# Kernel tuning notes

Hardware: AMD Instinct MI355X
Metric: run time of the kernel (lower is better)

## Reference

```python
import jax, jax.numpy as jnp
import numpy as np

N = 30000      # nodes
E = 480000     # edges (no self loops; GATConv adds them)
IN = 256       # in_features
OUT = 128      # out_features == per-head channels (concat=False)
H = 4          # heads
NEG_SLOPE = 0.2


def setup_inputs() -> dict:
    key = jax.random.key(0)
    k = jax.random.split(key, 6)
    x = jax.random.normal(k[0], (N, IN), dtype=jnp.float32)
    src = jax.random.randint(k[1], (E,), 0, N, dtype=jnp.int32)
    # guarantee no self loops (GATConv would strip them before re-adding)
    off = jax.random.randint(k[2], (E,), 1, N, dtype=jnp.int32)
    dst = (src + off) % N
    edge_index = jnp.stack([src, dst])  # [2, E]
    W = jax.random.normal(k[3], (IN, H * OUT), dtype=jnp.float32) / np.float32(np.sqrt(IN))
    att_src = jax.random.normal(k[4], (H, OUT), dtype=jnp.float32) / np.float32(np.sqrt(OUT))
    att_dst = jax.random.normal(k[5], (H, OUT), dtype=jnp.float32) / np.float32(np.sqrt(OUT))
    bias = jnp.zeros((OUT,), dtype=jnp.float32)
    return {"x": x, "edge_index": edge_index, "W": W,
            "att_src": att_src, "att_dst": att_dst, "bias": bias}


def reference(x, edge_index, W, att_src, att_dst, bias):
    n = x.shape[0]
    # dense projection -> per-head features [N, H, C]
    h = (x @ W).reshape(n, H, OUT)
    a_s = jnp.einsum('nhc,hc->nh', h, att_src)  # [N, H]
    a_d = jnp.einsum('nhc,hc->nh', h, att_dst)  # [N, H]
    # add self loops (GATConv default add_self_loops=True)
    loop = jnp.arange(n, dtype=edge_index.dtype)
    src = jnp.concatenate([edge_index[0], loop])  # [Et]
    dst = jnp.concatenate([edge_index[1], loop])  # [Et]
    # per-edge attention logits + LeakyReLU
    alpha = jax.nn.leaky_relu(a_s[src] + a_d[dst], NEG_SLOPE)  # [Et, H]
    # segment softmax over incoming edges of each dst node
    amax = jax.ops.segment_max(alpha, dst, num_segments=n)      # [N, H]
    ex = jnp.exp(alpha - amax[dst])
    denom = jax.ops.segment_sum(ex, dst, num_segments=n)        # [N, H]
    w = ex / denom[dst]                                          # [Et, H]
    # gather source features, weight, scatter-add to dst
    msg = h[src] * w[:, :, None]                                 # [Et, H, C]
    out = jax.ops.segment_sum(msg, dst, num_segments=n)          # [N, H, C]
    # concat=False -> mean over heads, then bias, then module's tanh
    out = out.mean(axis=1) + bias                                # [N, C]
    return jnp.tanh(out)
```

## Files before the change

### kernel.cpp

```cpp
#include <hip/hip_runtime.h>
#include <math.h>

#define IN_F   256
#define OUT_F  128
#define HEADS  4
#define HD     (HEADS * OUT_F)
#define NEG    0.2f
#define CAP    64

typedef __attribute__((ext_vector_type(8))) short short8;
typedef __attribute__((ext_vector_type(4))) float f32x4;

static __device__ __forceinline__ ushort f2bf(float f) {
    union { float f; unsigned u; } v; v.f = f;
    unsigned r = (v.u + 0x7FFFu + ((v.u >> 16) & 1u)) >> 16;
    return (ushort)r;
}
static __device__ __forceinline__ float bflo(unsigned u) {
    union { unsigned u; float f; } v; v.u = u << 16; return v.f;
}
static __device__ __forceinline__ float bfhi(unsigned u) {
    union { unsigned u; float f; } v; v.u = u & 0xFFFF0000u; return v.f;
}

__global__ __launch_bounds__(256) void cvt_wt(const float* __restrict__ W,
                                              ushort* __restrict__ WT) {
    int idx = blockIdx.x * blockDim.x + threadIdx.x;
    int n = idx >> 8, k = idx & 255;
    WT[idx] = f2bf(W[k * HD + n]);
}
__global__ __launch_bounds__(256) void calc_va(const float* __restrict__ W,
                                               const float* __restrict__ att_src,
                                               const float* __restrict__ att_dst,
                                               float* __restrict__ va_s,
                                               float* __restrict__ va_d) {
    int idx = blockIdx.x * blockDim.x + threadIdx.x;
    int h = idx >> 8, k = idx & 255;
    const float* wr = W + (size_t)k * HD + h * OUT_F;
    const float* as = att_src + h * OUT_F;
    const float* ad = att_dst + h * OUT_F;
    float ss = 0.f, sd = 0.f;
#pragma unroll 8
    for (int c = 0; c < OUT_F; ++c) {
        float w = wr[c];
        ss = fmaf(w, as[c], ss);
        sd = fmaf(w, ad[c], sd);
    }
    va_s[idx] = ss;
    va_d[idx] = sd;
}

__global__ __launch_bounds__(256) void fused_x(const float* __restrict__ X,
                                               const float* __restrict__ va_s,
                                               const float* __restrict__ va_d,
                                               ushort* __restrict__ Xb,
                                               float* __restrict__ a_s,
                                               float* __restrict__ a_d,
                                               int n_nodes) {
    const int lane = threadIdx.x & 63;
    const int node = blockIdx.x * 4 + (threadIdx.x >> 6);
    if (node >= n_nodes) return;
    float4 v = *(const float4*)(X + (size_t)node * IN_F + lane * 4);
    ushort4 o; o.x = f2bf(v.x); o.y = f2bf(v.y); o.z = f2bf(v.z); o.w = f2bf(v.w);
    *(ushort4*)(Xb + (size_t)node * IN_F + lane * 4) = o;

    float ps[HEADS], pd[HEADS];
#pragma unroll
    for (int hd = 0; hd < HEADS; ++hd) {
        float4 s4 = *(const float4*)(va_s + hd * IN_F + lane * 4);
        float4 d4 = *(const float4*)(va_d + hd * IN_F + lane * 4);
        ps[hd] = v.x * s4.x + v.y * s4.y + v.z * s4.z + v.w * s4.w;
        pd[hd] = v.x * d4.x + v.y * d4.y + v.z * d4.z + v.w * d4.w;
    }
#pragma unroll
    for (int off = 32; off > 0; off >>= 1) {
#pragma unroll
        for (int hd = 0; hd < HEADS; ++hd) {
            ps[hd] += __shfl_xor(ps[hd], off, 64);
            pd[hd] += __shfl_xor(pd[hd], off, 64);
        }
    }
    if (lane == 0) {
        float4 s4 = make_float4(ps[0], ps[1], ps[2], ps[3]);
        float4 d4 = make_float4(pd[0], pd[1], pd[2], pd[3]);
        *(float4*)(a_s + node * 4) = s4;
        *(float4*)(a_d + node * 4) = d4;
    }
}

#define GBM 128
#define GBN 128
#define GBK 32
#define LDA 40

__global__ __launch_bounds__(256) void gemm_mfma(const ushort* __restrict__ Xb,
                                                 const ushort* __restrict__ WT,
                                                 ushort* __restrict__ Hb,
                                                 int n_nodes) {
    __shared__ ushort As[GBM][LDA];
    __shared__ ushort Bs[GBN][LDA];
    const int tid = threadIdx.x;
    const int m0 = blockIdx.y * GBM;
    const int n0 = blockIdx.x * GBN;
    const int wave = tid >> 6, lane = tid & 63;
    const int wm = (wave & 1) * 64, wn = (wave >> 1) * 64;
    const int l15 = lane & 15, quad = lane >> 4;

    f32x4 acc[4][4];
#pragma unroll
    for (int i = 0; i < 4; ++i)
#pragma unroll
        for (int j = 0; j < 4; ++j) acc[i][j] = (f32x4){0.f, 0.f, 0.f, 0.f};

    const int r = tid >> 2, q = tid & 3;

    for (int k0 = 0; k0 < IN_F; k0 += GBK) {
        uint4 a0 = make_uint4(0, 0, 0, 0), a1 = a0;
        int gm0 = m0 + r, gm1 = m0 + 64 + r;
        if (gm0 < n_nodes) a0 = *(const uint4*)(Xb + (size_t)gm0 * IN_F + k0 + q * 8);
        if (gm1 < n_nodes) a1 = *(const uint4*)(Xb + (size_t)gm1 * IN_F + k0 + q * 8);
        uint4 b0 = *(const uint4*)(WT + (size_t)(n0 + r) * IN_F + k0 + q * 8);
        uint4 b1 = *(const uint4*)(WT + (size_t)(n0 + 64 + r) * IN_F + k0 + q * 8);
        __syncthreads();
        *(uint4*)&As[r][q * 8] = a0;
        *(uint4*)&As[64 + r][q * 8] = a1;
        *(uint4*)&Bs[r][q * 8] = b0;
        *(uint4*)&Bs[64 + r][q * 8] = b1;
        __syncthreads();

        short8 af[4], bf_[4];
#pragma unroll
        for (int f = 0; f < 4; ++f) {
            af[f]  = *(const short8*)&As[wm + f * 16 + l15][quad * 8];
            bf_[f] = *(const short8*)&Bs[wn + f * 16 + l15][quad * 8];
        }
#pragma unroll
        for (int fm = 0; fm < 4; ++fm)
#pragma unroll
            for (int fn = 0; fn < 4; ++fn)
                acc[fm][fn] = __builtin_amdgcn_mfma_f32_16x16x32_bf16(
                    af[fm], bf_[fn], acc[fm][fn], 0, 0, 0);
    }

#pragma unroll
    for (int fm = 0; fm < 4; ++fm) {
        int gmb = m0 + wm + fm * 16 + quad * 4;
#pragma unroll
        for (int reg = 0; reg < 4; ++reg) {
            int gm = gmb + reg;
            if (gm < n_nodes) {
#pragma unroll
                for (int fn = 0; fn < 4; ++fn)
                    Hb[(size_t)gm * HD + n0 + wn + fn * 16 + l15] =
                        f2bf(acc[fm][fn][reg]);
            }
        }
    }
}

__global__ __launch_bounds__(256) void build_table(const int* __restrict__ src,
                                                   const int* __restrict__ dst,
                                                   int* __restrict__ cursor,
                                                   int* __restrict__ table,
                                                   int n_edges) {
    int e = blockIdx.x * blockDim.x + threadIdx.x;
    if (e >= n_edges) return;
    int d = dst[e];
    int r = atomicAdd(&cursor[d], 1);
    if (r < CAP) table[(size_t)d * CAP + r] = src[e];
}

__global__ __launch_bounds__(256) void prep_weights(const float* __restrict__ a_s,
                                                    const float* __restrict__ a_d,
                                                    const int* __restrict__ cursor,
                                                    const int* __restrict__ table,
                                                    float* __restrict__ wtab,
                                                    float* __restrict__ wself,
                                                    float* __restrict__ rden,
                                                    int n_nodes) {
    const int lane = threadIdx.x & 63;
    const int n = blockIdx.x * 4 + (threadIdx.x >> 6);
    if (n >= n_nodes) return;
    int deg = cursor[n]; if (deg > CAP) deg = CAP;
    const int* row = table + (size_t)n * CAP;
    const float4 ad4 = *(const float4*)(a_d + n * 4);
    const float4 as4 = *(const float4*)(a_s + n * 4);
    const float ad[4] = {ad4.x, ad4.y, ad4.z, ad4.w};

    float aself[4];
    {
        const float asn[4] = {as4.x, as4.y, as4.z, as4.w};
#pragma unroll
        for (int hd = 0; hd < 4; ++hd) {
            float al = asn[hd] + ad[hd];
            aself[hd] = al > 0.f ? al : NEG * al;
        }
    }
    const bool act = lane < deg;
    float al[4];
    {
        int s = act ? row[lane] : 0;
        float4 av = act ? *(const float4*)(a_s + s * 4) : make_float4(0.f, 0.f, 0.f, 0.f);
        const float as_[4] = {av.x, av.y, av.z, av.w};
#pragma unroll
        for (int hd = 0; hd < 4; ++hd) {
            float a = as_[hd] + ad[hd];
            a = a > 0.f ? a : NEG * a;
            al[hd] = act ? a : -1e30f;
        }
    }
    float m[4];
#pragma unroll
    for (int hd = 0; hd < 4; ++hd) m[hd] = al[hd];
#pragma unroll
    for (int off = 32; off > 0; off >>= 1)
#pragma unroll
        for (int hd = 0; hd < 4; ++hd)
            m[hd] = fmaxf(m[hd], __shfl_xor(m[hd], off, 64));
#pragma unroll
    for (int hd = 0; hd < 4; ++hd) m[hd] = fmaxf(m[hd], aself[hd]);

    float w[4], den[4];
#pragma unroll
    for (int hd = 0; hd < 4; ++hd) {
        w[hd] = act ? __expf(al[hd] - m[hd]) : 0.f;
        den[hd] = w[hd];
    }
#pragma unroll
    for (int off = 32; off > 0; off >>= 1)
#pragma unroll
        for (int hd = 0; hd < 4; ++hd)
            den[hd] += __shfl_xor(den[hd], off, 64);

    if (act)
        *(float4*)(wtab + ((size_t)n * CAP + lane) * 4) =
            make_float4(w[0], w[1], w[2], w[3]);
    if (lane == 0) {
        float es[4];
        float4 ws, rd;
#pragma unroll
        for (int hd = 0; hd < 4; ++hd) es[hd] = __expf(aself[hd] - m[hd]);
        ws = make_float4(es[0], es[1], es[2], es[3]);
        rd = make_float4(1.f / (den[0] + es[0]), 1.f / (den[1] + es[1]),
                         1.f / (den[2] + es[2]), 1.f / (den[3] + es[3]));
        *(float4*)(wself + n * 4) = ws;
        *(float4*)(rden + n * 4) = rd;
    }
}

__global__ __launch_bounds__(256) void gat_agg(const ushort* __restrict__ Hb,
                                               const float* __restrict__ wtab,
                                               const float* __restrict__ wself,
                                               const float* __restrict__ rden,
                                               const int* __restrict__ cursor,
                                               const int* __restrict__ table,
                                               const float* __restrict__ bias,
                                               float* __restrict__ out) {
    const int lane = threadIdx.x & 63;
    const int n = blockIdx.x * 4 + (threadIdx.x >> 6);
    if (n >= 30000) return;
    int deg = cursor[n]; if (deg > CAP) deg = CAP;
    const int* row = table + (size_t)n * CAP;
    const float* wrow = wtab + (size_t)n * CAP * 4;
    const unsigned* hbase = (const unsigned*)Hb;

    float acc0[4], acc1[4];
    {
        const float4 ws = *(const float4*)(wself + n * 4);
        const float wsv[4] = {ws.x, ws.y, ws.z, ws.w};
        const unsigned* p = hbase + (size_t)n * 256;
#pragma unroll
        for (int hd = 0; hd < 4; ++hd) {
            unsigned u = p[hd * 64 + lane];
            acc0[hd] = wsv[hd] * bflo(u);
            acc1[hd] = wsv[hd] * bfhi(u);
        }
    }
    int e = 0;
    for (; e + 4 <= deg; e += 4) {
        int4 r4 = *(const int4*)(row + e);
        float4 w0 = *(const float4*)(wrow + (e + 0) * 4);
        float4 w1 = *(const float4*)(wrow + (e + 1) * 4);
        float4 w2 = *(const float4*)(wrow + (e + 2) * 4);
        float4 w3 = *(const float4*)(wrow + (e + 3) * 4);
        const unsigned* p0 = hbase + (size_t)r4.x * 256;
        const unsigned* p1 = hbase + (size_t)r4.y * 256;
        const unsigned* p2 = hbase + (size_t)r4.z * 256;
        const unsigned* p3 = hbase + (size_t)r4.w * 256;
        unsigned u0[4], u1[4], u2[4], u3[4];
#pragma unroll
        for (int hd = 0; hd < 4; ++hd) {
            u0[hd] = p0[hd * 64 + lane];
            u1[hd] = p1[hd * 64 + lane];
            u2[hd] = p2[hd * 64 + lane];
            u3[hd] = p3[hd * 64 + lane];
        }
        const float wv0[4] = {w0.x, w0.y, w0.z, w0.w};
        const float wv1[4] = {w1.x, w1.y, w1.z, w1.w};
        const float wv2[4] = {w2.x, w2.y, w2.z, w2.w};
        const float wv3[4] = {w3.x, w3.y, w3.z, w3.w};
#pragma unroll
        for (int hd = 0; hd < 4; ++hd) {
            acc0[hd] = fmaf(wv0[hd], bflo(u0[hd]), acc0[hd]);
            acc1[hd] = fmaf(wv0[hd], bfhi(u0[hd]), acc1[hd]);
            acc0[hd] = fmaf(wv1[hd], bflo(u1[hd]), acc0[hd]);
            acc1[hd] = fmaf(wv1[hd], bfhi(u1[hd]), acc1[hd]);
            acc0[hd] = fmaf(wv2[hd], bflo(u2[hd]), acc0[hd]);
            acc1[hd] = fmaf(wv2[hd], bfhi(u2[hd]), acc1[hd]);
            acc0[hd] = fmaf(wv3[hd], bflo(u3[hd]), acc0[hd]);
            acc1[hd] = fmaf(wv3[hd], bfhi(u3[hd]), acc1[hd]);
        }
    }
    for (; e < deg; ++e) {
        int s = row[e];
        float4 w = *(const float4*)(wrow + e * 4);
        const float wv[4] = {w.x, w.y, w.z, w.w};
        const unsigned* p = hbase + (size_t)s * 256;
#pragma unroll
        for (int hd = 0; hd < 4; ++hd) {
            unsigned u = p[hd * 64 + lane];
            acc0[hd] = fmaf(wv[hd], bflo(u), acc0[hd]);
            acc1[hd] = fmaf(wv[hd], bfhi(u), acc1[hd]);
        }
    }
    const float4 rd = *(const float4*)(rden + n * 4);
    const float rdv[4] = {rd.x, rd.y, rd.z, rd.w};
    float o0 = 0.f, o1 = 0.f;
#pragma unroll
    for (int hd = 0; hd < 4; ++hd) {
        o0 = fmaf(acc0[hd], rdv[hd], o0);
        o1 = fmaf(acc1[hd], rdv[hd], o1);
    }
    float2 b = *(const float2*)(bias + 2 * lane);
    o0 = 0.25f * o0 + b.x;
    o1 = 0.25f * o1 + b.y;
    float2 ov = make_float2(tanhf(o0), tanhf(o1));
    *(float2*)(out + (size_t)n * OUT_F + 2 * lane) = ov;
}

extern "C" void kernel_launch(void* const* d_in, const int* in_sizes, int n_in,
                              void* d_out, int out_size, void* d_ws, size_t ws_size,
                              hipStream_t stream) {
    const float* x       = (const float*)d_in[0];
    const int*   ei      = (const int*)d_in[1];
    const float* W       = (const float*)d_in[2];
    const float* att_src = (const float*)d_in[3];
    const float* att_dst = (const float*)d_in[4];
    const float* bias    = (const float*)d_in[5];
    float* out = (float*)d_out;

    const int n_nodes = in_sizes[0] / IN_F;
    const int n_edges = in_sizes[1] / 2;
    const int* src = ei;
    const int* dst = ei + n_edges;

    char* ws = (char*)d_ws;
    size_t off = 0;
    auto alloc = [&](size_t bytes) -> void* {
        void* p = ws + off;
        off = (off + bytes + 255) & ~(size_t)255;
        return p;
    };
    ushort* Hb     = (ushort*)alloc((size_t)n_nodes * HD * sizeof(ushort));
    ushort* Xb     = (ushort*)alloc((size_t)n_nodes * IN_F * sizeof(ushort));
    ushort* WT     = (ushort*)alloc((size_t)HD * IN_F * sizeof(ushort));
    float*  va_s   = (float*)alloc((size_t)HEADS * IN_F * sizeof(float));
    float*  va_d   = (float*)alloc((size_t)HEADS * IN_F * sizeof(float));
    float*  a_s    = (float*)alloc((size_t)n_nodes * HEADS * sizeof(float));
    float*  a_d    = (float*)alloc((size_t)n_nodes * HEADS * sizeof(float));
    int*    cursor = (int*)alloc((size_t)n_nodes * sizeof(int));
    int*    table  = (int*)alloc((size_t)n_nodes * CAP * sizeof(int));
    float*  wtab   = (float*)alloc((size_t)n_nodes * CAP * 4 * sizeof(float));
    float*  wself  = (float*)alloc((size_t)n_nodes * 4 * sizeof(float));
    float*  rden   = (float*)alloc((size_t)n_nodes * 4 * sizeof(float));
    (void)ws_size; (void)n_in; (void)out_size;

    hipMemsetAsync(cursor, 0, (size_t)n_nodes * sizeof(int), stream);

    cvt_wt<<<(HD * IN_F) / 256, 256, 0, stream>>>(W, WT);
    calc_va<<<(HEADS * IN_F) / 256, 256, 0, stream>>>(W, att_src, att_dst, va_s, va_d);
    fused_x<<<(n_nodes + 3) / 4, 256, 0, stream>>>(x, va_s, va_d, Xb, a_s, a_d, n_nodes);
    build_table<<<(n_edges + 255) / 256, 256, 0, stream>>>(src, dst, cursor, table, n_edges);

    dim3 ggrid(HD / GBN, (n_nodes + GBM - 1) / GBM);
    gemm_mfma<<<ggrid, 256, 0, stream>>>(Xb, WT, Hb, n_nodes);

    prep_weights<<<(n_nodes + 3) / 4, 256, 0, stream>>>(a_s, a_d, cursor, table,
                                                        wtab, wself, rden, n_nodes);
    gat_agg<<<(n_nodes + 3) / 4, 256, 0, stream>>>(Hb, wtab, wself, rden, cursor, table,
                                                   bias, out);
}
```

Before: 235.7 us.

## Fuse softmax weight prep into aggregation and use direct global-to-LDS loads in GEMM

Merges the prep_weights kernel into gat_agg, so each wave computes the per-edge softmax weights in registers and broadcasts them with shuffles. This removes the wtab, wself and rden round trips through global memory and one kernel launch. The GEMM now stages tiles with global_load_lds and an XOR-swizzled, unpadded LDS layout to avoid the register staging and bank conflicts. The gather loop is widened to 8 edges per iteration. The GEMM drops its row bounds checks on A and relies on Xb being placed first in the workspace so that out-of-range reads of the last tile stay inside valid memory.

```diff
diff --git a/kernel.cpp b/kernel.cpp
--- a/kernel.cpp
+++ b/kernel.cpp
@@ -10,6 +10,9 @@
 
 typedef __attribute__((ext_vector_type(8))) short short8;
 typedef __attribute__((ext_vector_type(4))) float f32x4;
+
+typedef __attribute__((address_space(1))) const void* gp_t;
+typedef __attribute__((address_space(3))) void* lp_t;
 
 static __device__ __forceinline__ ushort f2bf(float f) {
     union { float f; unsigned u; } v; v.f = f;
@@ -91,14 +94,13 @@
 #define GBM 128
 #define GBN 128
 #define GBK 32
-#define LDA 40
 
 __global__ __launch_bounds__(256) void gemm_mfma(const ushort* __restrict__ Xb,
                                                  const ushort* __restrict__ WT,
                                                  ushort* __restrict__ Hb,
                                                  int n_nodes) {
-    __shared__ ushort As[GBM][LDA];
-    __shared__ ushort Bs[GBN][LDA];
+    __shared__ ushort As[GBM][GBK];
+    __shared__ ushort Bs[GBN][GBK];
     const int tid = threadIdx.x;
     const int m0 = blockIdx.y * GBM;
     const int n0 = blockIdx.x * GBN;
@@ -106,33 +108,39 @@
     const int wm = (wave & 1) * 64, wn = (wave >> 1) * 64;
     const int l15 = lane & 15, quad = lane >> 4;
 
+    const int rr = lane >> 2;
+    const int cg = (lane & 3) ^ ((lane >> 3) & 3);
+    const int rA = wave * 16 + rr;
+    const ushort* gA0 = Xb + (size_t)(m0 + rA) * IN_F + cg * 8;
+    const ushort* gA1 = Xb + (size_t)(m0 + 64 + rA) * IN_F + cg * 8;
+    const ushort* gB0 = WT + (size_t)(n0 + rA) * IN_F + cg * 8;
+    const ushort* gB1 = WT + (size_t)(n0 + 64 + rA) * IN_F + cg * 8;
+    ushort* lA0 = &As[wave * 16][0];
+    ushort* lA1 = &As[64 + wave * 16][0];
+    ushort* lB0 = &Bs[wave * 16][0];
+    ushort* lB1 = &Bs[64 + wave * 16][0];
+
     f32x4 acc[4][4];
 #pragma unroll
     for (int i = 0; i < 4; ++i)
 #pragma unroll
         for (int j = 0; j < 4; ++j) acc[i][j] = (f32x4){0.f, 0.f, 0.f, 0.f};
 
-    const int r = tid >> 2, q = tid & 3;
+    const int ks = (quad ^ ((l15 >> 1) & 3)) * 8;
 
     for (int k0 = 0; k0 < IN_F; k0 += GBK) {
-        uint4 a0 = make_uint4(0, 0, 0, 0), a1 = a0;
-        int gm0 = m0 + r, gm1 = m0 + 64 + r;
-        if (gm0 < n_nodes) a0 = *(const uint4*)(Xb + (size_t)gm0 * IN_F + k0 + q * 8);
-        if (gm1 < n_nodes) a1 = *(const uint4*)(Xb + (size_t)gm1 * IN_F + k0 + q * 8);
-        uint4 b0 = *(const uint4*)(WT + (size_t)(n0 + r) * IN_F + k0 + q * 8);
-        uint4 b1 = *(const uint4*)(WT + (size_t)(n0 + 64 + r) * IN_F + k0 + q * 8);
         __syncthreads();
-        *(uint4*)&As[r][q * 8] = a0;
-        *(uint4*)&As[64 + r][q * 8] = a1;
-        *(uint4*)&Bs[r][q * 8] = b0;
-        *(uint4*)&Bs[64 + r][q * 8] = b1;
+        __builtin_amdgcn_global_load_lds((gp_t)(gA0 + k0), (lp_t)lA0, 16, 0, 0);
+        __builtin_amdgcn_global_load_lds((gp_t)(gA1 + k0), (lp_t)lA1, 16, 0, 0);
+        __builtin_amdgcn_global_load_lds((gp_t)(gB0 + k0), (lp_t)lB0, 16, 0, 0);
+        __builtin_amdgcn_global_load_lds((gp_t)(gB1 + k0), (lp_t)lB1, 16, 0, 0);
         __syncthreads();
 
         short8 af[4], bf_[4];
 #pragma unroll
         for (int f = 0; f < 4; ++f) {
-            af[f]  = *(const short8*)&As[wm + f * 16 + l15][quad * 8];
-            bf_[f] = *(const short8*)&Bs[wn + f * 16 + l15][quad * 8];
+            af[f]  = *(const short8*)&As[wm + f * 16 + l15][ks];
+            bf_[f] = *(const short8*)&Bs[wn + f * 16 + l15][ks];
         }
 #pragma unroll
         for (int fm = 0; fm < 4; ++fm)
@@ -170,23 +178,24 @@
     if (r < CAP) table[(size_t)d * CAP + r] = src[e];
 }
 
-__global__ __launch_bounds__(256) void prep_weights(const float* __restrict__ a_s,
-                                                    const float* __restrict__ a_d,
-                                                    const int* __restrict__ cursor,
-                                                    const int* __restrict__ table,
-                                                    float* __restrict__ wtab,
-                                                    float* __restrict__ wself,
-                                                    float* __restrict__ rden,
-                                                    int n_nodes) {
+__global__ __launch_bounds__(256) void gat_agg(const ushort* __restrict__ Hb,
+                                               const float* __restrict__ a_s,
+                                               const float* __restrict__ a_d,
+                                               const int* __restrict__ cursor,
+                                               const int* __restrict__ table,
+                                               const float* __restrict__ bias,
+                                               float* __restrict__ out,
+                                               int n_nodes) {
     const int lane = threadIdx.x & 63;
     const int n = blockIdx.x * 4 + (threadIdx.x >> 6);
     if (n >= n_nodes) return;
     int deg = cursor[n]; if (deg > CAP) deg = CAP;
     const int* row = table + (size_t)n * CAP;
+    const unsigned* hbase = (const unsigned*)Hb;
+
     const float4 ad4 = *(const float4*)(a_d + n * 4);
     const float4 as4 = *(const float4*)(a_s + n * 4);
     const float ad[4] = {ad4.x, ad4.y, ad4.z, ad4.w};
-
     float aself[4];
     {
         const float asn[4] = {as4.x, as4.y, as4.z, as4.w};
@@ -200,7 +209,7 @@
     float al[4];
     {
         int s = act ? row[lane] : 0;
-        float4 av = act ? *(const float4*)(a_s + s * 4) : make_float4(0.f, 0.f, 0.f, 0.f);
+        float4 av = *(const float4*)(a_s + s * 4);
         const float as_[4] = {av.x, av.y, av.z, av.w};
 #pragma unroll
         for (int hd = 0; hd < 4; ++hd) {
@@ -220,7 +229,7 @@
 #pragma unroll
     for (int hd = 0; hd < 4; ++hd) m[hd] = fmaxf(m[hd], aself[hd]);
 
-    float w[4], den[4];
+    float w[4], den[4], es[4];
 #pragma unroll
     for (int hd = 0; hd < 4; ++hd) {
         w[hd] = act ? __expf(al[hd] - m[hd]) : 0.f;
@@ -231,100 +240,59 @@
 #pragma unroll
         for (int hd = 0; hd < 4; ++hd)
             den[hd] += __shfl_xor(den[hd], off, 64);
-
-    if (act)
-        *(float4*)(wtab + ((size_t)n * CAP + lane) * 4) =
-            make_float4(w[0], w[1], w[2], w[3]);
-    if (lane == 0) {
-        float es[4];
-        float4 ws, rd;
-#pragma unroll
-        for (int hd = 0; hd < 4; ++hd) es[hd] = __expf(aself[hd] - m[hd]);
-        ws = make_float4(es[0], es[1], es[2], es[3]);
-        rd = make_float4(1.f / (den[0] + es[0]), 1.f / (den[1] + es[1]),
-                         1.f / (den[2] + es[2]), 1.f / (den[3] + es[3]));
-        *(float4*)(wself + n * 4) = ws;
-        *(float4*)(rden + n * 4) = rd;
-    }
-}
-
-__global__ __launch_bounds__(256) void gat_agg(const ushort* __restrict__ Hb,
-                                               const float* __restrict__ wtab,
-                                               const float* __restrict__ wself,
-                                               const float* __restrict__ rden,
-                                               const int* __restrict__ cursor,
-                                               const int* __restrict__ table,
-                                               const float* __restrict__ bias,
-                                               float* __restrict__ out) {
-    const int lane = threadIdx.x & 63;
-    const int n = blockIdx.x * 4 + (threadIdx.x >> 6);
-    if (n >= 30000) return;
-    int deg = cursor[n]; if (deg > CAP) deg = CAP;
-    const int* row = table + (size_t)n * CAP;
-    const float* wrow = wtab + (size_t)n * CAP * 4;
-    const unsigned* hbase = (const unsigned*)Hb;
+    float rdv[4];
+#pragma unroll
+    for (int hd = 0; hd < 4; ++hd) {
+        es[hd] = __expf(aself[hd] - m[hd]);
+        rdv[hd] = 1.f / (den[hd] + es[hd]);
+    }
 
     float acc0[4], acc1[4];
     {
-        const float4 ws = *(const float4*)(wself + n * 4);
-        const float wsv[4] = {ws.x, ws.y, ws.z, ws.w};
         const unsigned* p = hbase + (size_t)n * 256;
 #pragma unroll
         for (int hd = 0; hd < 4; ++hd) {
             unsigned u = p[hd * 64 + lane];
-            acc0[hd] = wsv[hd] * bflo(u);
-            acc1[hd] = wsv[hd] * bfhi(u);
+            acc0[hd] = es[hd] * bflo(u);
+            acc1[hd] = es[hd] * bfhi(u);
         }
     }
     int e = 0;
-    for (; e + 4 <= deg; e += 4) {
-        int4 r4 = *(const int4*)(row + e);
-        float4 w0 = *(const float4*)(wrow + (e + 0) * 4);
-        float4 w1 = *(const float4*)(wrow + (e + 1) * 4);
-        float4 w2 = *(const float4*)(wrow + (e + 2) * 4);
-        float4 w3 = *(const float4*)(wrow + (e + 3) * 4);
-        const unsigned* p0 = hbase + (size_t)r4.x * 256;
-        const unsigned* p1 = hbase + (size_t)r4.y * 256;
-        const unsigned* p2 = hbase + (size_t)r4.z * 256;
-        const unsigned* p3 = hbase + (size_t)r4.w * 256;
-        unsigned u0[4], u1[4], u2[4], u3[4];
-#pragma unroll
-        for (int hd = 0; hd < 4; ++hd) {
-            u0[hd] = p0[hd * 64 + lane];
-            u1[hd] = p1[hd * 64 + lane];
-            u2[hd] = p2[hd * 64 + lane];
-            u3[hd] = p3[hd * 64 + lane];
-        }
-        const float wv0[4] = {w0.x, w0.y, w0.z, w0.w};
-        const float wv1[4] = {w1.x, w1.y, w1.z, w1.w};
-        const float wv2[4] = {w2.x, w2.y, w2.z, w2.w};
-        const float wv3[4] = {w3.x, w3.y, w3.z, w3.w};
-#pragma unroll
-        for (int hd = 0; hd < 4; ++hd) {
-            acc0[hd] = fmaf(wv0[hd], bflo(u0[hd]), acc0[hd]);
-            acc1[hd] = fmaf(wv0[hd], bfhi(u0[hd]), acc1[hd]);
-            acc0[hd] = fmaf(wv1[hd], bflo(u1[hd]), acc0[hd]);
-            acc1[hd] = fmaf(wv1[hd], bfhi(u1[hd]), acc1[hd]);
-            acc0[hd] = fmaf(wv2[hd], bflo(u2[hd]), acc0[hd]);
-            acc1[hd] = fmaf(wv2[hd], bfhi(u2[hd]), acc1[hd]);
-            acc0[hd] = fmaf(wv3[hd], bflo(u3[hd]), acc0[hd]);
-            acc1[hd] = fmaf(wv3[hd], bfhi(u3[hd]), acc1[hd]);
+    for (; e + 8 <= deg; e += 8) {
+        int4 ra = *(const int4*)(row + e);
+        int4 rb = *(const int4*)(row + e + 4);
+        const unsigned* p[8];
+        p[0] = hbase + (size_t)ra.x * 256; p[1] = hbase + (size_t)ra.y * 256;
+        p[2] = hbase + (size_t)ra.z * 256; p[3] = hbase + (size_t)ra.w * 256;
+        p[4] = hbase + (size_t)rb.x * 256; p[5] = hbase + (size_t)rb.y * 256;
+        p[6] = hbase + (size_t)rb.z * 256; p[7] = hbase + (size_t)rb.w * 256;
+        unsigned u[8][4];
+#pragma unroll
+        for (int j = 0; j < 8; ++j)
+#pragma unroll
+            for (int hd = 0; hd < 4; ++hd)
+                u[j][hd] = p[j][hd * 64 + lane];
+#pragma unroll
+        for (int j = 0; j < 8; ++j) {
+#pragma unroll
+            for (int hd = 0; hd < 4; ++hd) {
+                float wv = __shfl(w[hd], e + j, 64);
+                acc0[hd] = fmaf(wv, bflo(u[j][hd]), acc0[hd]);
+                acc1[hd] = fmaf(wv, bfhi(u[j][hd]), acc1[hd]);
+            }
         }
     }
     for (; e < deg; ++e) {
         int s = row[e];
-        float4 w = *(const float4*)(wrow + e * 4);
-        const float wv[4] = {w.x, w.y, w.z, w.w};
         const unsigned* p = hbase + (size_t)s * 256;
 #pragma unroll
         for (int hd = 0; hd < 4; ++hd) {
             unsigned u = p[hd * 64 + lane];
-            acc0[hd] = fmaf(wv[hd], bflo(u), acc0[hd]);
-            acc1[hd] = fmaf(wv[hd], bfhi(u), acc1[hd]);
-        }
-    }
-    const float4 rd = *(const float4*)(rden + n * 4);
-    const float rdv[4] = {rd.x, rd.y, rd.z, rd.w};
+            float wv = __shfl(w[hd], e, 64);
+            acc0[hd] = fmaf(wv, bflo(u), acc0[hd]);
+            acc1[hd] = fmaf(wv, bfhi(u), acc1[hd]);
+        }
+    }
     float o0 = 0.f, o1 = 0.f;
 #pragma unroll
     for (int hd = 0; hd < 4; ++hd) {
@@ -361,8 +329,8 @@
         off = (off + bytes + 255) & ~(size_t)255;
         return p;
     };
+    ushort* Xb     = (ushort*)alloc((size_t)n_nodes * IN_F * sizeof(ushort));
     ushort* Hb     = (ushort*)alloc((size_t)n_nodes * HD * sizeof(ushort));
-    ushort* Xb     = (ushort*)alloc((size_t)n_nodes * IN_F * sizeof(ushort));
     ushort* WT     = (ushort*)alloc((size_t)HD * IN_F * sizeof(ushort));
     float*  va_s   = (float*)alloc((size_t)HEADS * IN_F * sizeof(float));
     float*  va_d   = (float*)alloc((size_t)HEADS * IN_F * sizeof(float));
@@ -370,9 +338,6 @@
     float*  a_d    = (float*)alloc((size_t)n_nodes * HEADS * sizeof(float));
     int*    cursor = (int*)alloc((size_t)n_nodes * sizeof(int));
     int*    table  = (int*)alloc((size_t)n_nodes * CAP * sizeof(int));
-    float*  wtab   = (float*)alloc((size_t)n_nodes * CAP * 4 * sizeof(float));
-    float*  wself  = (float*)alloc((size_t)n_nodes * 4 * sizeof(float));
-    float*  rden   = (float*)alloc((size_t)n_nodes * 4 * sizeof(float));
     (void)ws_size; (void)n_in; (void)out_size;
 
     hipMemsetAsync(cursor, 0, (size_t)n_nodes * sizeof(int), stream);
@@ -385,8 +350,6 @@
     dim3 ggrid(HD / GBN, (n_nodes + GBM - 1) / GBM);
     gemm_mfma<<<ggrid, 256, 0, stream>>>(Xb, WT, Hb, n_nodes);
 
-    prep_weights<<<(n_nodes + 3) / 4, 256, 0, stream>>>(a_s, a_d, cursor, table,
-                                                        wtab, wself, rden, n_nodes);
-    gat_agg<<<(n_nodes + 3) / 4, 256, 0, stream>>>(Hb, wtab, wself, rden, cursor, table,
-                                                   bias, out);
-}
+    gat_agg<<<(n_nodes + 3) / 4, 256, 0, stream>>>(Hb, a_s, a_d, cursor, table,
+                                                   bias, out, n_nodes);
+}
```

Result: faster. 229.9 us (-2.5%).

## Load GEMM tiles directly into LDS with XOR swizzle; shrink aggregation blocks

Applied to the files above, without the earlier changes.

The GEMM now stages its A/B tiles with global_load_lds, which writes global data straight into shared memory and skips the register round-trip. The padded LDS layout is replaced by an XOR-swizzled one to avoid bank conflicts. The bounds check on rows is dropped, which is why Xb is now allocated before Hb, so the tail block's over-read of Xb lands in Hb's buffer instead of past the end. prep_weights and gat_agg move from 256-thread to 128-thread blocks, and gat_agg takes n_nodes as a parameter instead of a hardcoded count.

```diff
diff --git a/kernel.cpp b/kernel.cpp
--- a/kernel.cpp
+++ b/kernel.cpp
@@ -10,6 +10,9 @@
 
 typedef __attribute__((ext_vector_type(8))) short short8;
 typedef __attribute__((ext_vector_type(4))) float f32x4;
+
+typedef __attribute__((address_space(1))) const void* gp_t;
+typedef __attribute__((address_space(3))) void* lp_t;
 
 static __device__ __forceinline__ ushort f2bf(float f) {
     union { float f; unsigned u; } v; v.f = f;
@@ -91,14 +94,13 @@
 #define GBM 128
 #define GBN 128
 #define GBK 32
-#define LDA 40
 
 __global__ __launch_bounds__(256) void gemm_mfma(const ushort* __restrict__ Xb,
                                                  const ushort* __restrict__ WT,
                                                  ushort* __restrict__ Hb,
                                                  int n_nodes) {
-    __shared__ ushort As[GBM][LDA];
-    __shared__ ushort Bs[GBN][LDA];
+    __shared__ ushort As[GBM][GBK];
+    __shared__ ushort Bs[GBN][GBK];
     const int tid = threadIdx.x;
     const int m0 = blockIdx.y * GBM;
     const int n0 = blockIdx.x * GBN;
@@ -106,33 +108,39 @@
     const int wm = (wave & 1) * 64, wn = (wave >> 1) * 64;
     const int l15 = lane & 15, quad = lane >> 4;
 
+    const int rr = lane >> 2;
+    const int cg = (lane & 3) ^ ((lane >> 3) & 3);
+    const int rA = wave * 16 + rr;
+    const ushort* gA0 = Xb + (size_t)(m0 + rA) * IN_F + cg * 8;
+    const ushort* gA1 = Xb + (size_t)(m0 + 64 + rA) * IN_F + cg * 8;
+    const ushort* gB0 = WT + (size_t)(n0 + rA) * IN_F + cg * 8;
+    const ushort* gB1 = WT + (size_t)(n0 + 64 + rA) * IN_F + cg * 8;
+    ushort* lA0 = &As[wave * 16][0];
+    ushort* lA1 = &As[64 + wave * 16][0];
+    ushort* lB0 = &Bs[wave * 16][0];
+    ushort* lB1 = &Bs[64 + wave * 16][0];
+
     f32x4 acc[4][4];
 #pragma unroll
     for (int i = 0; i < 4; ++i)
 #pragma unroll
         for (int j = 0; j < 4; ++j) acc[i][j] = (f32x4){0.f, 0.f, 0.f, 0.f};
 
-    const int r = tid >> 2, q = tid & 3;
+    const int ks = (quad ^ ((l15 >> 1) & 3)) * 8;
 
     for (int k0 = 0; k0 < IN_F; k0 += GBK) {
-        uint4 a0 = make_uint4(0, 0, 0, 0), a1 = a0;
-        int gm0 = m0 + r, gm1 = m0 + 64 + r;
-        if (gm0 < n_nodes) a0 = *(const uint4*)(Xb + (size_t)gm0 * IN_F + k0 + q * 8);
-        if (gm1 < n_nodes) a1 = *(const uint4*)(Xb + (size_t)gm1 * IN_F + k0 + q * 8);
-        uint4 b0 = *(const uint4*)(WT + (size_t)(n0 + r) * IN_F + k0 + q * 8);
-        uint4 b1 = *(const uint4*)(WT + (size_t)(n0 + 64 + r) * IN_F + k0 + q * 8);
         __syncthreads();
-        *(uint4*)&As[r][q * 8] = a0;
-        *(uint4*)&As[64 + r][q * 8] = a1;
-        *(uint4*)&Bs[r][q * 8] = b0;
-        *(uint4*)&Bs[64 + r][q * 8] = b1;
+        __builtin_amdgcn_global_load_lds((gp_t)(gA0 + k0), (lp_t)lA0, 16, 0, 0);
+        __builtin_amdgcn_global_load_lds((gp_t)(gA1 + k0), (lp_t)lA1, 16, 0, 0);
+        __builtin_amdgcn_global_load_lds((gp_t)(gB0 + k0), (lp_t)lB0, 16, 0, 0);
+        __builtin_amdgcn_global_load_lds((gp_t)(gB1 + k0), (lp_t)lB1, 16, 0, 0);
         __syncthreads();
 
         short8 af[4], bf_[4];
 #pragma unroll
         for (int f = 0; f < 4; ++f) {
-            af[f]  = *(const short8*)&As[wm + f * 16 + l15][quad * 8];
-            bf_[f] = *(const short8*)&Bs[wn + f * 16 + l15][quad * 8];
+            af[f]  = *(const short8*)&As[wm + f * 16 + l15][ks];
+            bf_[f] = *(const short8*)&Bs[wn + f * 16 + l15][ks];
         }
 #pragma unroll
         for (int fm = 0; fm < 4; ++fm)
@@ -170,7 +178,7 @@
     if (r < CAP) table[(size_t)d * CAP + r] = src[e];
 }
 
-__global__ __launch_bounds__(256) void prep_weights(const float* __restrict__ a_s,
+__global__ __launch_bounds__(128) void prep_weights(const float* __restrict__ a_s,
                                                     const float* __restrict__ a_d,
                                                     const int* __restrict__ cursor,
                                                     const int* __restrict__ table,
@@ -179,7 +187,7 @@
                                                     float* __restrict__ rden,
                                                     int n_nodes) {
     const int lane = threadIdx.x & 63;
-    const int n = blockIdx.x * 4 + (threadIdx.x >> 6);
+    const int n = blockIdx.x * 2 + (threadIdx.x >> 6);
     if (n >= n_nodes) return;
     int deg = cursor[n]; if (deg > CAP) deg = CAP;
     const int* row = table + (size_t)n * CAP;
@@ -200,7 +208,7 @@
     float al[4];
     {
         int s = act ? row[lane] : 0;
-        float4 av = act ? *(const float4*)(a_s + s * 4) : make_float4(0.f, 0.f, 0.f, 0.f);
+        float4 av = *(const float4*)(a_s + s * 4);
         const float as_[4] = {av.x, av.y, av.z, av.w};
 #pragma unroll
         for (int hd = 0; hd < 4; ++hd) {
@@ -237,28 +245,27 @@
             make_float4(w[0], w[1], w[2], w[3]);
     if (lane == 0) {
         float es[4];
-        float4 ws, rd;
 #pragma unroll
         for (int hd = 0; hd < 4; ++hd) es[hd] = __expf(aself[hd] - m[hd]);
-        ws = make_float4(es[0], es[1], es[2], es[3]);
-        rd = make_float4(1.f / (den[0] + es[0]), 1.f / (den[1] + es[1]),
-                         1.f / (den[2] + es[2]), 1.f / (den[3] + es[3]));
-        *(float4*)(wself + n * 4) = ws;
-        *(float4*)(rden + n * 4) = rd;
-    }
-}
-
-__global__ __launch_bounds__(256) void gat_agg(const ushort* __restrict__ Hb,
+        *(float4*)(wself + n * 4) = make_float4(es[0], es[1], es[2], es[3]);
+        *(float4*)(rden + n * 4) =
+            make_float4(1.f / (den[0] + es[0]), 1.f / (den[1] + es[1]),
+                        1.f / (den[2] + es[2]), 1.f / (den[3] + es[3]));
+    }
+}
+
+__global__ __launch_bounds__(128) void gat_agg(const ushort* __restrict__ Hb,
                                                const float* __restrict__ wtab,
                                                const float* __restrict__ wself,
                                                const float* __restrict__ rden,
                                                const int* __restrict__ cursor,
                                                const int* __restrict__ table,
                                                const float* __restrict__ bias,
-                                               float* __restrict__ out) {
+                                               float* __restrict__ out,
+                                               int n_nodes) {
     const int lane = threadIdx.x & 63;
-    const int n = blockIdx.x * 4 + (threadIdx.x >> 6);
-    if (n >= 30000) return;
+    const int n = blockIdx.x * 2 + (threadIdx.x >> 6);
+    if (n >= n_nodes) return;
     int deg = cursor[n]; if (deg > CAP) deg = CAP;
     const int* row = table + (size_t)n * CAP;
     const float* wrow = wtab + (size_t)n * CAP * 4;
@@ -361,8 +368,8 @@
         off = (off + bytes + 255) & ~(size_t)255;
         return p;
     };
+    ushort* Xb     = (ushort*)alloc((size_t)n_nodes * IN_F * sizeof(ushort));
     ushort* Hb     = (ushort*)alloc((size_t)n_nodes * HD * sizeof(ushort));
-    ushort* Xb     = (ushort*)alloc((size_t)n_nodes * IN_F * sizeof(ushort));
     ushort* WT     = (ushort*)alloc((size_t)HD * IN_F * sizeof(ushort));
     float*  va_s   = (float*)alloc((size_t)HEADS * IN_F * sizeof(float));
     float*  va_d   = (float*)alloc((size_t)HEADS * IN_F * sizeof(float));
@@ -385,8 +392,8 @@
     dim3 ggrid(HD / GBN, (n_nodes + GBM - 1) / GBM);
     gemm_mfma<<<ggrid, 256, 0, stream>>>(Xb, WT, Hb, n_nodes);
 
-    prep_weights<<<(n_nodes + 3) / 4, 256, 0, stream>>>(a_s, a_d, cursor, table,
+    prep_weights<<<(n_nodes + 1) / 2, 128, 0, stream>>>(a_s, a_d, cursor, table,
                                                         wtab, wself, rden, n_nodes);
-    gat_agg<<<(n_nodes + 3) / 4, 256, 0, stream>>>(Hb, wtab, wself, rden, cursor, table,
-                                                   bias, out);
-}
+    gat_agg<<<(n_nodes + 1) / 2, 128, 0, stream>>>(Hb, wtab, wself, rden, cursor, table,
+                                                   bias, out, n_nodes);
+}
```

New measurement: 238.0 us. About the same (+1.0%).
